# Kernel optimization log

Hardware: AMD Instinct MI355X
Metric: run time of the kernel (lower is better)

The kernel has to match this reference:

```python
import jax, jax.numpy as jnp
import numpy as np


def _laplacian(x, edge_src, edge_dst, n_nodes):
    # x: [B, N, C]; L[:, i, :] = x[:, i, :] - mean over neighbors j of x[:, j, :]
    # (nodes with zero neighbors get L = 0, matching the torch loop which skips them)
    xt = jnp.transpose(x, (1, 0, 2))                      # [N, B, C]
    gathered = xt[edge_src]                               # [E, B, C]
    neigh_sum = jax.ops.segment_sum(gathered, edge_dst, num_segments=n_nodes)  # [N, B, C]
    deg = jax.ops.segment_sum(jnp.ones_like(edge_dst, dtype=x.dtype), edge_dst,
                              num_segments=n_nodes)       # [N]
    safe_deg = jnp.maximum(deg, 1.0)
    neigh_mean = neigh_sum / safe_deg[:, None, None]
    lap = jnp.where(deg[:, None, None] > 0, xt - neigh_mean, jnp.zeros((), x.dtype))
    return jnp.transpose(lap, (1, 0, 2))                  # [B, N, C]


def setup_inputs() -> dict:
    key = jax.random.key(0)
    k1, k2, k3, k4 = jax.random.split(key, 4)
    B, N, C = 4, 100000, 32
    E = 1600000  # avg degree 16
    pred = jax.random.normal(k1, (B, N, C), dtype=jnp.float32)
    target = jax.random.normal(k2, (B, N, C), dtype=jnp.float32)
    edge_src = jax.random.randint(k3, (E,), 0, N, dtype=jnp.int32)
    edge_dst = jax.random.randint(k4, (E,), 0, N, dtype=jnp.int32)
    return {"pred": pred, "target": target, "edge_src": edge_src, "edge_dst": edge_dst}


def reference(pred, target, edge_src, edge_dst):
    n_nodes = pred.shape[1]
    lap_pred = _laplacian(pred, edge_src, edge_dst, n_nodes)
    lap_target = _laplacian(target, edge_src, edge_dst, n_nodes)
    # nn.L1Loss() default reduction='mean' over all elements
    return jnp.mean(jnp.abs(lap_pred - lap_target))
```

## Files before the change

kernel.cpp:

```cpp
#include <hip/hip_runtime.h>
#include <hip/hip_bf16.h>
#include <cmath>

#define BB 4
#define CC 32

#define KMAX   512
#define NSUBMAX (KMAX * 4)

#if __has_builtin(__builtin_amdgcn_cvt_pk_f32_bf8) && __has_builtin(__builtin_amdgcn_cvt_pk_bf8_f32)
#define HW_BF8 1
typedef float f2v __attribute__((ext_vector_type(2)));
#else
#define HW_BF8 0
#endif

__device__ __forceinline__ unsigned pack_bf2(float x, float y) {
    unsigned bx = __float_as_uint(x); bx += 0x7fffu + ((bx >> 16) & 1u);
    unsigned by = __float_as_uint(y); by += 0x7fffu + ((by >> 16) & 1u);
    return (bx >> 16) | (by & 0xffff0000u);
}

__device__ __forceinline__ unsigned pack_e5(float x) {
    _Float16 h = (_Float16)x;
    unsigned hb = (unsigned)__builtin_bit_cast(unsigned short, h);
    hb += 0x7fu + ((hb >> 8) & 1u);
    return (hb >> 8) & 0xffu;
}

__device__ __forceinline__ float e5h(unsigned hw) {
    return (float)__builtin_bit_cast(_Float16, (unsigned short)hw);
}

__device__ __forceinline__ unsigned pack_e5x4(float d0, float d1, float d2, float d3) {
#if HW_BF8
    int w = __builtin_amdgcn_cvt_pk_bf8_f32(d0, d1, 0, false);
    w     = __builtin_amdgcn_cvt_pk_bf8_f32(d2, d3, w, true);
    return (unsigned)w;
#else
    return pack_e5(d0) | (pack_e5(d1) << 8) | (pack_e5(d2) << 16) | (pack_e5(d3) << 24);
#endif
}

__device__ __forceinline__ void acc_e5(float* acc, uint2 v) {
#if HW_BF8
    f2v p0 = __builtin_amdgcn_cvt_pk_f32_bf8((int)v.x, false);
    f2v p1 = __builtin_amdgcn_cvt_pk_f32_bf8((int)v.x, true);
    f2v p2 = __builtin_amdgcn_cvt_pk_f32_bf8((int)v.y, false);
    f2v p3 = __builtin_amdgcn_cvt_pk_f32_bf8((int)v.y, true);
    acc[0] += p0[0]; acc[1] += p0[1];
    acc[2] += p1[0]; acc[3] += p1[1];
    acc[4] += p2[0]; acc[5] += p2[1];
    acc[6] += p3[0]; acc[7] += p3[1];
#else
    unsigned a = v.x, b = v.y;
    acc[0] += e5h((a << 8) & 0xff00u);
    acc[1] += e5h(a & 0xff00u);
    acc[2] += e5h((a >> 8) & 0xff00u);
    acc[3] += e5h((a >> 16) & 0xff00u);
    acc[4] += e5h((b << 8) & 0xff00u);
    acc[5] += e5h(b & 0xff00u);
    acc[6] += e5h((b >> 8) & 0xff00u);
    acc[7] += e5h((b >> 16) & 0xff00u);
#endif
}

__global__ __launch_bounds__(1024) void prep_a(
        const float* __restrict__ pred, const float* __restrict__ target,
        const int* __restrict__ edge_src, const int* __restrict__ edge_dst,
        int* __restrict__ bucketCursor, unsigned* __restrict__ staged,
        unsigned* __restrict__ diffu, unsigned* __restrict__ diffu8,
        int N, int E, int buildBlocks, int K, int sstride) {
    if ((int)blockIdx.x < buildBlocks) {
        __shared__ int cnt[NSUBMAX];
        __shared__ int base[NSUBMAX];
        int nsub = K << 2;
        for (int k = threadIdx.x; k < nsub; k += 1024) cnt[k] = 0;
        __syncthreads();
        int e0 = blockIdx.x * 8192;
        unsigned w[8]; int rp[8];
        #pragma unroll
        for (int t = 0; t < 8; ++t) {
            int i = e0 + t * 1024 + threadIdx.x;
            if (i < E) {
                int d = edge_dst[i];
                int s = edge_src[i];
                int sbk = d >> 6;
                w[t] = (unsigned)s | ((unsigned)(d & 63) << 17);
                int r = atomicAdd(&cnt[sbk], 1);
                rp[t] = r | (sbk << 13);
            } else rp[t] = -1;
        }
        __syncthreads();
        for (int k = threadIdx.x; k < nsub; k += 1024) {
            int c = cnt[k];
            base[k] = c ? atomicAdd(&bucketCursor[k], c) : 0;
        }
        __syncthreads();
        #pragma unroll
        for (int t = 0; t < 8; ++t) {
            if (rp[t] >= 0) {
                int sbk = rp[t] >> 13;
                int pos = base[sbk] + (rp[t] & 8191);
                if (pos < sstride)
                    staged[(size_t)sbk * sstride + pos] = w[t];
            }
        }
    } else {
        int idx4 = ((int)blockIdx.x - buildBlocks) * 1024 + threadIdx.x;
        int total4 = N * CC;
        if (idx4 < total4) {
            int n8 = N * 8;
            int b  = idx4 / n8;
            int r  = idx4 - b * n8;
            int n  = r >> 3;
            const float4 p = *(const float4*)(pred   + ((size_t)idx4 << 2));
            const float4 t = *(const float4*)(target + ((size_t)idx4 << 2));
            float d0 = p.x - t.x, d1 = p.y - t.y, d2 = p.z - t.z, d3 = p.w - t.w;
            uint2 u;
            u.x = pack_bf2(d0, d1);
            u.y = pack_bf2(d2, d3);
            *(uint2*)(diffu + (size_t)n * 64 + b * 16 + ((r & 7) << 1)) = u;
            diffu8[(size_t)n * 32 + b * 8 + (r & 7)] = pack_e5x4(d0, d1, d2, d3);
        }
    }
}

__global__ __launch_bounds__(256) void node_gather(
        const unsigned* __restrict__ diffu, const unsigned* __restrict__ diffu8,
        const unsigned* __restrict__ staged,
        const int* __restrict__ bucketCursor, float* __restrict__ partials,
        int N, int sstride) {
    __shared__ int lists[64 * 65];
    __shared__ int cnt[64];
    __shared__ float wpart[4];

    int subg = blockIdx.x;
    if (threadIdx.x < 64) cnt[threadIdx.x] = 0;
    __syncthreads();

    int count = min(bucketCursor[subg], sstride);
    const unsigned* sb = staged + (size_t)subg * sstride;
    for (int i = threadIdx.x; i < count; i += 256) {
        unsigned wv = sb[i];
        int l = (wv >> 17) & 63;
        int slot = atomicAdd(&cnt[l], 1);
        if (slot < 64) lists[l * 65 + slot] = wv & 0x1ffff;
    }
    __syncthreads();

    int wave = threadIdx.x >> 6;
    int lane = threadIdx.x & 63;
    int q  = lane >> 4;
    int l4 = lane & 15;
    const unsigned* base16 = diffu  + l4 * 4;
    const unsigned* base8  = diffu8 + l4 * 2;
    int node0 = subg << 6;
    float total = 0.0f;

    for (int tt = 0; tt < 4; ++tt) {
        int lslot = (wave << 4) + (tt << 2) + q;
        int node  = node0 + lslot;
        int d = (node < N) ? min(cnt[lslot], 64) : 0;
        if (d > 0) {
            int dm1   = d - 1;
            int lbase = lslot * 65;
            uint4 su = *(const uint4*)(base16 + (size_t)node * 64);

            float accA[8], accB[8];
            #pragma unroll
            for (int k = 0; k < 8; ++k) { accA[k] = 0.f; accB[k] = 0.f; }

            for (int j = 0; j < d; j += 4) {
                int s0 = lists[lbase + j];
                int s1 = lists[lbase + min(j + 1, dm1)];
                int s2 = lists[lbase + min(j + 2, dm1)];
                int s3 = lists[lbase + min(j + 3, dm1)];
                uint2 v0 = *(const uint2*)(base8 + (size_t)s0 * 32);
                uint2 v1 = *(const uint2*)(base8 + (size_t)s1 * 32);
                uint2 v2 = *(const uint2*)(base8 + (size_t)s2 * 32);
                uint2 v3 = *(const uint2*)(base8 + (size_t)s3 * 32);
                acc_e5(accA, v0);
                if (j + 1 < d) acc_e5(accB, v1);
                if (j + 2 < d) acc_e5(accA, v2);
                if (j + 3 < d) acc_e5(accB, v3);
            }

            float inv = 1.0f / (float)d;
            const unsigned* sp = (const unsigned*)&su;
            #pragma unroll
            for (int k = 0; k < 8; ++k) {
                float v = accA[k] + accB[k];
                unsigned spk = sp[k >> 1];
                float s = (k & 1) ? __uint_as_float(spk & 0xffff0000u)
                                  : __uint_as_float(spk << 16);
                total += fabsf(s - v * inv);
            }
        }
    }
    #pragma unroll
    for (int delta = 32; delta >= 1; delta >>= 1)
        total += __shfl_down(total, delta, 64);
    if (lane == 0) wpart[wave] = total;
    __syncthreads();
    if (threadIdx.x == 0)
        partials[blockIdx.x] = wpart[0] + wpart[1] + wpart[2] + wpart[3];
}

__global__ __launch_bounds__(256) void reduce_kernel(const float* __restrict__ partials, int n,
                                                     float* __restrict__ out, float inv_count) {
    float s = 0.0f;
    for (int i = threadIdx.x; i < n; i += 256) s += partials[i];
    int lane = threadIdx.x & 63;
    int wave = threadIdx.x >> 6;
    #pragma unroll
    for (int delta = 32; delta >= 1; delta >>= 1)
        s += __shfl_down(s, delta, 64);
    __shared__ float wpart[4];
    if (lane == 0) wpart[wave] = s;
    __syncthreads();
    if (threadIdx.x == 0)
        out[0] = (wpart[0] + wpart[1] + wpart[2] + wpart[3]) * inv_count;
}

__global__ void build_kernel(const int* __restrict__ edge_src, const int* __restrict__ edge_dst,
                             int* __restrict__ deg, int* __restrict__ csr, int E) {
    int i = blockIdx.x * 256 + threadIdx.x;
    if (i < E) {
        int d = edge_dst[i];
        int slot = atomicAdd(&deg[d], 1);
        if (slot < 64) csr[(d << 6) + slot] = edge_src[i];
    }
}

__global__ __launch_bounds__(256) void node_kernel_pt(const float* __restrict__ pred,
                                                      const float* __restrict__ target,
                                                      const int* __restrict__ csr,
                                                      const int* __restrict__ deg,
                                                      float* __restrict__ partials, int N) {
    int wave = threadIdx.x >> 6;
    int lane = threadIdx.x & 63;
    int node = blockIdx.x * 4 + wave;
    float total = 0.0f;
    if (node < N) {
        int d = min(deg[node], 64);
        if (d > 0) {
            int o = node << 6;
            int cs = csr[o + lane];
            int b = (lane >> 3) & 3;
            int q = lane & 7;
            const float* arr = (lane >= 32) ? target : pred;
            int rowbase = b * N * CC + q * 4;
            float4 sp = *(const float4*)(pred + rowbase + node * CC);
            float4 st = *(const float4*)(target + rowbase + node * CC);
            float ax = 0.f, ay = 0.f, az = 0.f, aw = 0.f;
            for (int j = 0; j < d; ++j) {
                int s = __shfl(cs, j, 64);
                float4 v = *(const float4*)(arr + rowbase + s * CC);
                ax += v.x; ay += v.y; az += v.z; aw += v.w;
            }
            float dx = ax - __shfl_down(ax, 32, 64);
            float dy = ay - __shfl_down(ay, 32, 64);
            float dz = az - __shfl_down(az, 32, 64);
            float dw = aw - __shfl_down(aw, 32, 64);
            if (lane < 32) {
                float inv = 1.0f / (float)d;
                total = fabsf((sp.x - st.x) - dx * inv)
                      + fabsf((sp.y - st.y) - dy * inv)
                      + fabsf((sp.z - st.z) - dz * inv)
                      + fabsf((sp.w - st.w) - dw * inv);
            }
        }
    }
    #pragma unroll
    for (int delta = 32; delta >= 1; delta >>= 1)
        total += __shfl_down(total, delta, 64);
    __shared__ float wpart[4];
    if (lane == 0) wpart[wave] = total;
    __syncthreads();
    if (threadIdx.x == 0)
        partials[blockIdx.x] = wpart[0] + wpart[1] + wpart[2] + wpart[3];
}

extern "C" void kernel_launch(void* const* d_in, const int* in_sizes, int n_in,
                              void* d_out, int out_size, void* d_ws, size_t ws_size,
                              hipStream_t stream) {
    const float* pred   = (const float*)d_in[0];
    const float* target = (const float*)d_in[1];
    const int* edge_src = (const int*)d_in[2];
    const int* edge_dst = (const int*)d_in[3];
    float* out = (float*)d_out;

    const int BNC = in_sizes[0];
    const int E   = in_sizes[2];
    const int N   = BNC / (BB * CC);
    const int K   = (N + 255) >> 8;
    const int nsub = 4 * K;

    const int msub = E / nsub + 1;
    const int sstride = msub + 8 * (int)sqrtf((float)msub) + 64;

    size_t staged_off = NSUBMAX;
    size_t diff_off   = staged_off + (size_t)nsub * sstride;
    diff_off = (diff_off + 3) & ~(size_t)3;
    size_t diff8_off  = diff_off + ((size_t)N << 6);
    size_t part_off   = diff8_off + ((size_t)N << 5);
    size_t fast_bytes = (part_off + (size_t)nsub + 16) * 4;

    if (ws_size >= fast_bytes && N <= 131072 && K <= KMAX) {
        int* cursor = (int*)d_ws;
        unsigned* staged = (unsigned*)((int*)d_ws + staged_off);
        unsigned* diffu  = (unsigned*)((int*)d_ws + diff_off);
        unsigned* diffu8 = (unsigned*)((int*)d_ws + diff8_off);
        float* partials  = (float*)((int*)d_ws + part_off);

        hipMemsetAsync(cursor, 0, NSUBMAX * sizeof(int), stream);
        const int buildBlocks = (E + 8191) / 8192;
        const int diffBlocks  = (N * CC + 1023) / 1024;
        prep_a<<<buildBlocks + diffBlocks, 1024, 0, stream>>>(
            pred, target, edge_src, edge_dst, cursor, staged, diffu, diffu8,
            N, E, buildBlocks, K, sstride);
        node_gather<<<nsub, 256, 0, stream>>>(diffu, diffu8, staged, cursor,
                                              partials, N, sstride);
        reduce_kernel<<<1, 256, 0, stream>>>(partials, nsub, out, 1.0f / (float)BNC);
    } else {
        int* deg = (int*)d_ws;
        int* csr = deg + N;
        float* partials = (float*)(csr + ((size_t)N << 6));
        const int nblocks4 = (N + 3) / 4;

        hipMemsetAsync(deg, 0, (size_t)N * sizeof(int), stream);
        const int eblocks = (E + 255) / 256;
        build_kernel<<<eblocks, 256, 0, stream>>>(edge_src, edge_dst, deg, csr, E);
        node_kernel_pt<<<nblocks4, 256, 0, stream>>>(pred, target, csr, deg, partials, N);
        reduce_kernel<<<1, 256, 0, stream>>>(partials, nblocks4, out, 1.0f / (float)BNC);
    }
}
```

Baseline: 187.2 us.

## Drop bf16 self-diff buffer and fuse final reduction via atomics

Stops writing the bf16 packed self-difference buffer in the prep kernel; the gather kernel now reads the node's own pred and target rows directly in fp32 and computes the difference there. The separate reduce kernel is removed: each gather block atomically adds its scaled partial sum into the output, which prep_a zeroes first. This saves one buffer write, one launch and the partials pass, in exchange for strided fp32 reads of the self term, float atomics with nondeterministic ordering, and a dependence on prep_a running before node_gather.

New measurement: 208.0 us. 1.11x slower.

```diff
diff --git a/kernel.cpp b/kernel.cpp
--- a/kernel.cpp
+++ b/kernel.cpp
@@ -14,12 +14,6 @@
 #else
 #define HW_BF8 0
 #endif
-
-__device__ __forceinline__ unsigned pack_bf2(float x, float y) {
-    unsigned bx = __float_as_uint(x); bx += 0x7fffu + ((bx >> 16) & 1u);
-    unsigned by = __float_as_uint(y); by += 0x7fffu + ((by >> 16) & 1u);
-    return (bx >> 16) | (by & 0xffff0000u);
-}
 
 __device__ __forceinline__ unsigned pack_e5(float x) {
     _Float16 h = (_Float16)x;
@@ -69,8 +63,9 @@
         const float* __restrict__ pred, const float* __restrict__ target,
         const int* __restrict__ edge_src, const int* __restrict__ edge_dst,
         int* __restrict__ bucketCursor, unsigned* __restrict__ staged,
-        unsigned* __restrict__ diffu, unsigned* __restrict__ diffu8,
+        unsigned* __restrict__ diffu8, float* __restrict__ outz,
         int N, int E, int buildBlocks, int K, int sstride) {
+    if (blockIdx.x == 0 && threadIdx.x == 0) *outz = 0.0f;
     if ((int)blockIdx.x < buildBlocks) {
         __shared__ int cnt[NSUBMAX];
         __shared__ int base[NSUBMAX];
@@ -116,21 +111,17 @@
             int n  = r >> 3;
             const float4 p = *(const float4*)(pred   + ((size_t)idx4 << 2));
             const float4 t = *(const float4*)(target + ((size_t)idx4 << 2));
-            float d0 = p.x - t.x, d1 = p.y - t.y, d2 = p.z - t.z, d3 = p.w - t.w;
-            uint2 u;
-            u.x = pack_bf2(d0, d1);
-            u.y = pack_bf2(d2, d3);
-            *(uint2*)(diffu + (size_t)n * 64 + b * 16 + ((r & 7) << 1)) = u;
-            diffu8[(size_t)n * 32 + b * 8 + (r & 7)] = pack_e5x4(d0, d1, d2, d3);
+            diffu8[(size_t)n * 32 + b * 8 + (r & 7)] =
+                pack_e5x4(p.x - t.x, p.y - t.y, p.z - t.z, p.w - t.w);
         }
     }
 }
 
 __global__ __launch_bounds__(256) void node_gather(
-        const unsigned* __restrict__ diffu, const unsigned* __restrict__ diffu8,
-        const unsigned* __restrict__ staged,
-        const int* __restrict__ bucketCursor, float* __restrict__ partials,
-        int N, int sstride) {
+        const float* __restrict__ pred, const float* __restrict__ target,
+        const unsigned* __restrict__ diffu8, const unsigned* __restrict__ staged,
+        const int* __restrict__ bucketCursor, float* __restrict__ out,
+        int N, int sstride, float inv_count) {
     __shared__ int lists[64 * 65];
     __shared__ int cnt[64];
     __shared__ float wpart[4];
@@ -153,8 +144,9 @@
     int lane = threadIdx.x & 63;
     int q  = lane >> 4;
     int l4 = lane & 15;
-    const unsigned* base16 = diffu  + l4 * 4;
-    const unsigned* base8  = diffu8 + l4 * 2;
+    const unsigned* base8 = diffu8 + l4 * 2;
+    const float* pbase = pred   + (size_t)(l4 >> 2) * N * CC + ((l4 & 3) << 3);
+    const float* tbase = target + (size_t)(l4 >> 2) * N * CC + ((l4 & 3) << 3);
     int node0 = subg << 6;
     float total = 0.0f;
 
@@ -165,7 +157,10 @@
         if (d > 0) {
             int dm1   = d - 1;
             int lbase = lslot * 65;
-            uint4 su = *(const uint4*)(base16 + (size_t)node * 64);
+            const float4* pp = (const float4*)(pbase + (size_t)node * CC);
+            const float4* tp = (const float4*)(tbase + (size_t)node * CC);
+            float4 p0 = pp[0], p1 = pp[1];
+            float4 t0 = tp[0], t1 = tp[1];
 
             float accA[8], accB[8];
             #pragma unroll
@@ -187,15 +182,18 @@
             }
 
             float inv = 1.0f / (float)d;
-            const unsigned* sp = (const unsigned*)&su;
-            #pragma unroll
-            for (int k = 0; k < 8; ++k) {
-                float v = accA[k] + accB[k];
-                unsigned spk = sp[k >> 1];
-                float s = (k & 1) ? __uint_as_float(spk & 0xffff0000u)
-                                  : __uint_as_float(spk << 16);
-                total += fabsf(s - v * inv);
-            }
+            float s0f = p0.x - t0.x, s1f = p0.y - t0.y;
+            float s2f = p0.z - t0.z, s3f = p0.w - t0.w;
+            float s4f = p1.x - t1.x, s5f = p1.y - t1.y;
+            float s6f = p1.z - t1.z, s7f = p1.w - t1.w;
+            total += fabsf(s0f - (accA[0] + accB[0]) * inv)
+                   + fabsf(s1f - (accA[1] + accB[1]) * inv)
+                   + fabsf(s2f - (accA[2] + accB[2]) * inv)
+                   + fabsf(s3f - (accA[3] + accB[3]) * inv)
+                   + fabsf(s4f - (accA[4] + accB[4]) * inv)
+                   + fabsf(s5f - (accA[5] + accB[5]) * inv)
+                   + fabsf(s6f - (accA[6] + accB[6]) * inv)
+                   + fabsf(s7f - (accA[7] + accB[7]) * inv);
         }
     }
     #pragma unroll
@@ -204,7 +202,7 @@
     if (lane == 0) wpart[wave] = total;
     __syncthreads();
     if (threadIdx.x == 0)
-        partials[blockIdx.x] = wpart[0] + wpart[1] + wpart[2] + wpart[3];
+        atomicAdd(out, (wpart[0] + wpart[1] + wpart[2] + wpart[3]) * inv_count);
 }
 
 __global__ __launch_bounds__(256) void reduce_kernel(const float* __restrict__ partials, int n,
@@ -301,28 +299,24 @@
     const int sstride = msub + 8 * (int)sqrtf((float)msub) + 64;
 
     size_t staged_off = NSUBMAX;
-    size_t diff_off   = staged_off + (size_t)nsub * sstride;
-    diff_off = (diff_off + 3) & ~(size_t)3;
-    size_t diff8_off  = diff_off + ((size_t)N << 6);
-    size_t part_off   = diff8_off + ((size_t)N << 5);
-    size_t fast_bytes = (part_off + (size_t)nsub + 16) * 4;
+    size_t diff8_off  = staged_off + (size_t)nsub * sstride;
+    diff8_off = (diff8_off + 3) & ~(size_t)3;
+    size_t fast_bytes = (diff8_off + ((size_t)N << 5) + 16) * 4;
 
     if (ws_size >= fast_bytes && N <= 131072 && K <= KMAX) {
         int* cursor = (int*)d_ws;
         unsigned* staged = (unsigned*)((int*)d_ws + staged_off);
-        unsigned* diffu  = (unsigned*)((int*)d_ws + diff_off);
         unsigned* diffu8 = (unsigned*)((int*)d_ws + diff8_off);
-        float* partials  = (float*)((int*)d_ws + part_off);
 
         hipMemsetAsync(cursor, 0, NSUBMAX * sizeof(int), stream);
         const int buildBlocks = (E + 8191) / 8192;
         const int diffBlocks  = (N * CC + 1023) / 1024;
         prep_a<<<buildBlocks + diffBlocks, 1024, 0, stream>>>(
-            pred, target, edge_src, edge_dst, cursor, staged, diffu, diffu8,
+            pred, target, edge_src, edge_dst, cursor, staged, diffu8, out,
             N, E, buildBlocks, K, sstride);
-        node_gather<<<nsub, 256, 0, stream>>>(diffu, diffu8, staged, cursor,
-                                              partials, N, sstride);
-        reduce_kernel<<<1, 256, 0, stream>>>(partials, nsub, out, 1.0f / (float)BNC);
+        node_gather<<<nsub, 256, 0, stream>>>(pred, target, diffu8, staged,
+                                              cursor, out, N, sstride,
+                                              1.0f / (float)BNC);
     } else {
         int* deg = (int*)d_ws;
         int* csr = deg + N;
```
